# Kernel tuning notes

Hardware: AMD Instinct MI355X
Metric: run time of the kernel (lower is better)

Reference implementation:

```python
import jax, jax.numpy as jnp
import numpy as np

HID = 4096
NH = 32
NKV = 8
HD = 128
ROPE_BASE = 1000000.0
EPS = 1e-6
Q_SIZE = NH * HD      # 4096
KV_SIZE = NKV * HD    # 1024


def rms_norm(x, w):
    # x: [..., HD]
    var = jnp.mean(x * x, axis=-1, keepdims=True)
    return x * jax.lax.rsqrt(var + EPS) * w


def apply_rope(x, cos, sin):
    # x: [T, H, HD], cos/sin: [T, 1, HD//2]; neox-style rotate-half
    x1, x2 = jnp.split(x, 2, axis=-1)
    return jnp.concatenate([x1 * cos - x2 * sin, x2 * cos + x1 * sin], axis=-1)


def setup_inputs() -> dict:
    key = jax.random.key(0)
    ks = jax.random.split(key, 8)
    T = 4096
    inp = {
        "positions": jnp.arange(T, dtype=jnp.int32),
        "hidden_states": jax.random.normal(ks[0], (T, HID), dtype=jnp.float32),
        "ctx_len": 3072,
        "w_qkv": jax.random.normal(ks[1], (HID, Q_SIZE + 2 * KV_SIZE), dtype=jnp.float32) * 0.02,
        "b_qkv": jax.random.normal(ks[2], (Q_SIZE + 2 * KV_SIZE,), dtype=jnp.float32) * 0.02,
        "q_norm_w": 1.0 + 0.02 * jax.random.normal(ks[3], (HD,), dtype=jnp.float32),
        "k_norm_w": 1.0 + 0.02 * jax.random.normal(ks[4], (HD,), dtype=jnp.float32),
        "w_o": jax.random.normal(ks[5], (Q_SIZE, HID), dtype=jnp.float32) * 0.02,
    }
    return inp


def reference(positions, hidden_states, ctx_len, w_qkv, b_qkv, q_norm_w, k_norm_w, w_o):
    T = hidden_states.shape[0]
    noise_len = T - ctx_len

    qkv = hidden_states @ w_qkv + b_qkv                     # [T, 6144]
    q = qkv[:, :Q_SIZE].reshape(T, NH, HD)
    k = qkv[:, Q_SIZE:Q_SIZE + KV_SIZE].reshape(T, NKV, HD)
    v = qkv[:, Q_SIZE + KV_SIZE:].reshape(T, NKV, HD)

    # per-head RMSNorm on q and k
    q = rms_norm(q, q_norm_w)
    k = rms_norm(k, k_norm_w)

    # RoPE (neox style, full rotary dim)
    half = HD // 2
    inv_freq = 1.0 / (ROPE_BASE ** (jnp.arange(half, dtype=jnp.float32) / half))
    freqs = positions.astype(jnp.float32)[:, None] * inv_freq[None, :]   # [T, half]
    cos = jnp.cos(freqs)[:, None, :]
    sin = jnp.sin(freqs)[:, None, :]
    q = apply_rope(q, cos, sin)
    k = apply_rope(k, cos, sin)

    # Q from noise positions only; K/V from full sequence (non-causal)
    qn = q[ctx_len:]                                        # [N, NH, HD]
    g = NH // NKV
    qn = qn.reshape(noise_len, NKV, g, HD)                  # [N, kv, g, HD]
    scale = HD ** -0.5

    # scores: [kv, g, N, T] in fp32 (faithful to fp32 softmax)
    scores = jnp.einsum("nkgd,tkd->kgnt", qn, k) * scale
    probs = jax.nn.softmax(scores.astype(jnp.float32), axis=-1).astype(v.dtype)
    out = jnp.einsum("kgnt,tkd->nkgd", probs, v)            # [N, kv, g, HD]
    out = out.reshape(noise_len, NH * HD)
    return out @ w_o                                        # [N, HID]
```

## Files before the change

kernel.cpp:

```cpp
#include <hip/hip_runtime.h>
#include <stdint.h>

#define NH 32
#define NKV 8
#define HD 128
#define HID 4096
#define NQKV 6144

typedef __attribute__((ext_vector_type(8))) __bf16 bf16x8;
typedef __attribute__((ext_vector_type(4))) float f32x4;
typedef __attribute__((ext_vector_type(4))) float float4v;
typedef __attribute__((ext_vector_type(8))) unsigned short ushort8v;
typedef __attribute__((ext_vector_type(4))) unsigned short ushort4v;
typedef __attribute__((ext_vector_type(2))) unsigned short ushort2v;

__device__ __forceinline__ unsigned short f2bf(float f) {
  union { float f; unsigned u; } x; x.f = f;
  unsigned r = x.u + 0x7fffu + ((x.u >> 16) & 1u);
  return (unsigned short)(r >> 16);
}

__device__ __forceinline__ void gld16(const void* g, void* l) {
  __builtin_amdgcn_global_load_lds(
      (const __attribute__((address_space(1))) unsigned int*)g,
      (__attribute__((address_space(3))) unsigned int*)l, 16, 0, 0);
}

__device__ __forceinline__ f32x4 mfma16(bf16x8 a, bf16x8 b, f32x4 c) {
  return __builtin_amdgcn_mfma_f32_16x16x32_bf16(a, b, c, 0, 0, 0);
}

__global__ void ropetab(const int* __restrict__ pos, float* __restrict__ cosT,
                        float* __restrict__ sinT) {
  const int t = blockIdx.x, f = threadIdx.x;
  const double inv = exp(-0.2158673524681918 * (double)f);
  const double arg = (double)pos[t] * inv;
  cosT[t * 64 + f] = (float)cos(arg);
  sinT[t * 64 + f] = (float)sin(arg);
}

__global__ void convbf(const float* __restrict__ src, unsigned short* __restrict__ dst,
                       long n4) {
  long i = (long)blockIdx.x * blockDim.x + threadIdx.x;
  const long stride = (long)gridDim.x * blockDim.x;
  for (; i < n4; i += stride) {
    float4v v = *(const float4v*)(src + i * 4);
    ushort4v o;
    o.x = f2bf(v.x); o.y = f2bf(v.y); o.z = f2bf(v.z); o.w = f2bf(v.w);
    *(ushort4v*)(dst + i * 4) = o;
  }
}

__global__ __launch_bounds__(256) void wtrans(const float* __restrict__ W,
                                              unsigned short* __restrict__ Wt,
                                              int K, int N) {
  __shared__ float tile[64][65];
  const int k0 = blockIdx.y * 64, n0 = blockIdx.x * 64;
  const int tid = threadIdx.x;
  const int rk = tid >> 4, cn = (tid & 15) * 4;
#pragma unroll
  for (int rr = 0; rr < 64; rr += 16) {
    float4v v = *(const float4v*)(W + (long)(k0 + rk + rr) * N + n0 + cn);
    tile[rk + rr][cn] = v.x; tile[rk + rr][cn + 1] = v.y;
    tile[rk + rr][cn + 2] = v.z; tile[rk + rr][cn + 3] = v.w;
  }
  __syncthreads();
  const int rn = tid >> 3, ck = (tid & 7) * 8;
#pragma unroll
  for (int rr = 0; rr < 64; rr += 32) {
    ushort8v o;
#pragma unroll
    for (int j = 0; j < 8; ++j) o[j] = f2bf(tile[ck + j][rn + rr]);
    *(ushort8v*)(Wt + (long)(n0 + rn + rr) * K + k0 + ck) = o;
  }
}

__global__ __launch_bounds__(256) void vtrans(const float* __restrict__ qkv,
                                              unsigned short* __restrict__ Vt, int T) {
  __shared__ float tile[64][65];
  const int kvh = blockIdx.z;
  const int t0 = blockIdx.x * 64, d0 = blockIdx.y * 64;
  const int tid = threadIdx.x;
  const int rt = tid >> 4, cd = (tid & 15) * 4;
#pragma unroll
  for (int rr = 0; rr < 64; rr += 16) {
    float4v v = *(const float4v*)(qkv + (long)(t0 + rt + rr) * NQKV + 5120 + kvh * 128 + d0 + cd);
    tile[rt + rr][cd] = v.x; tile[rt + rr][cd + 1] = v.y;
    tile[rt + rr][cd + 2] = v.z; tile[rt + rr][cd + 3] = v.w;
  }
  __syncthreads();
  const int rd = tid >> 3, ct = (tid & 7) * 8;
#pragma unroll
  for (int rr = 0; rr < 64; rr += 32) {
    ushort8v o;
#pragma unroll
    for (int j = 0; j < 8; ++j) o[j] = f2bf(tile[ct + j][rd + rr]);
    *(ushort8v*)(Vt + ((long)kvh * 128 + d0 + rd + rr) * T + t0 + ct) = o;
  }
}

__global__ __launch_bounds__(256) void norm_rope(
    const float* __restrict__ qkv, const float* __restrict__ qw,
    const float* __restrict__ kw, const float* __restrict__ cosT,
    const float* __restrict__ sinT, unsigned short* __restrict__ Qo,
    unsigned short* __restrict__ Ko, int T, int ctx, int noise) {
  const int t = blockIdx.x;
  __shared__ float cs[64], sn[64];
  const int tid = threadIdx.x;
  if (tid < 64) { cs[tid] = cosT[t * 64 + tid]; sn[tid] = sinT[t * 64 + tid]; }
  __syncthreads();
  const int wid = tid >> 6, lane = tid & 63;
  const float* row = qkv + (long)t * NQKV;
  const bool isNoise = (t >= ctx);
  for (int sl = wid; sl < 40; sl += 4) {
    if (sl < 32 && !isNoise) continue;
    const float* x = row + sl * 128;
    float v0 = x[lane * 2], v1 = x[lane * 2 + 1];
    float ss = v0 * v0 + v1 * v1;
#pragma unroll
    for (int off = 32; off >= 1; off >>= 1) ss += __shfl_xor(ss, off);
    const float rinv = rsqrtf(ss * (1.f / 128.f) + 1e-6f);
    const float* w = (sl < 32) ? qw : kw;
    v0 *= rinv * w[lane * 2];
    v1 *= rinv * w[lane * 2 + 1];
    const float p0 = __shfl_xor(v0, 32);
    const float p1 = __shfl_xor(v1, 32);
    const int f0 = (lane * 2) & 63, f1 = (lane * 2 + 1) & 63;
    float o0, o1;
    if (lane < 32) { o0 = v0 * cs[f0] - p0 * sn[f0]; o1 = v1 * cs[f1] - p1 * sn[f1]; }
    else           { o0 = v0 * cs[f0] + p0 * sn[f0]; o1 = v1 * cs[f1] + p1 * sn[f1]; }
    ushort2v o; o.x = f2bf(o0); o.y = f2bf(o1);
    if (sl < 32)
      *(ushort2v*)(Qo + ((long)sl * noise + (t - ctx)) * 128 + lane * 2) = o;
    else
      *(ushort2v*)(Ko + ((long)(sl - 32) * T + t) * 128 + lane * 2) = o;
  }
}

__global__ __launch_bounds__(256) void gemm_qkv(
    const unsigned short* __restrict__ A, const unsigned short* __restrict__ Bt,
    float* __restrict__ C, const float* __restrict__ bias, int ctx, int nKV) {
  __shared__ unsigned short As[2][128 * 32];
  __shared__ unsigned short Bs[2][128 * 32];
  const int K = HID;
  const int tid = threadIdx.x;
  const int wid = tid >> 6, lane = tid & 63;
  const int lr = lane & 15, lg = lane >> 4;
  const int cpx = gridDim.x >> 3;
  const int swz = (blockIdx.x & 7) * cpx + (blockIdx.x >> 3);
  long bm, bn;
  if (swz < nKV) {
    bm = (long)(swz / 16) * 128;
    bn = 4096 + (long)(swz % 16) * 128;
  } else {
    const int r = swz - nKV;
    bm = ctx + (long)(r / 48) * 128;
    bn = (long)(r % 48) * 128;
  }
  const int wm = (wid >> 1) * 64;
  const int wn = (wid & 1) * 64;
  f32x4 acc[4][4] = {};

  const int r0 = (wid * 64 + lane) >> 2;
  const int ce0 = ((wid * 64 + lane) & 3) * 8;
  const int r1 = ((4 + wid) * 64 + lane) >> 2;
  const int ce1 = (((4 + wid) * 64 + lane) & 3) * 8;

#define STAGE(buf, k0)                                                        \
  do {                                                                        \
    gld16(A + (bm + r0) * (long)K + (k0) + ce0, As[buf] + wid * 512);         \
    gld16(Bt + (bn + r0) * (long)K + (k0) + ce0, Bs[buf] + wid * 512);        \
    gld16(A + (bm + r1) * (long)K + (k0) + ce1, As[buf] + (4 + wid) * 512);   \
    gld16(Bt + (bn + r1) * (long)K + (k0) + ce1, Bs[buf] + (4 + wid) * 512);  \
  } while (0)

#define COMPUTE(buf)                                                          \
  do {                                                                        \
    bf16x8 af[4], bfv[4];                                                     \
    _Pragma("unroll") for (int i = 0; i < 4; ++i) {                           \
      af[i]  = *(const bf16x8*)(As[buf] + (wm + i * 16 + lr) * 32 + lg * 8);  \
      bfv[i] = *(const bf16x8*)(Bs[buf] + (wn + i * 16 + lr) * 32 + lg * 8);  \
    }                                                                         \
    _Pragma("unroll") for (int i = 0; i < 4; ++i)                             \
      _Pragma("unroll") for (int j = 0; j < 4; ++j)                           \
        acc[i][j] = mfma16(af[i], bfv[j], acc[i][j]);                         \
  } while (0)

  STAGE(0, 0);
  __syncthreads();
  int cur = 0;
  for (int k0 = 32; k0 < K; k0 += 32) {
    STAGE(cur ^ 1, k0);
    COMPUTE(cur);
    __syncthreads();
    cur ^= 1;
  }
  COMPUTE(cur);

#pragma unroll
  for (int i = 0; i < 4; ++i) {
#pragma unroll
    for (int j = 0; j < 4; ++j) {
      const long row = bm + wm + i * 16 + lg * 4;
      const long col = bn + wn + j * 16 + lr;
      const float b = bias[col];
#pragma unroll
      for (int r = 0; r < 4; ++r)
        C[(row + r) * (long)NQKV + col] = acc[i][j][r] + b;
    }
  }
}

__global__ __launch_bounds__(256) void gemm_bt(
    const unsigned short* __restrict__ A, const unsigned short* __restrict__ Bt,
    float* __restrict__ C, int M, int N, int K) {
  __shared__ unsigned short As[2][128 * 32];
  __shared__ unsigned short Bs[2][128 * 32];
  const int tid = threadIdx.x;
  const int wid = tid >> 6, lane = tid & 63;
  const int lr = lane & 15, lg = lane >> 4;
  const long bm = (long)blockIdx.y * 128;
  const long bn = (long)blockIdx.x * 128;
  const int wm = (wid >> 1) * 64;
  const int wn = (wid & 1) * 64;
  const int kLen = K / gridDim.z;
  const int kOff = blockIdx.z * kLen;
  float* Cz = C + (size_t)blockIdx.z * M * N;
  f32x4 acc[4][4] = {};

  const int r0 = (wid * 64 + lane) >> 2;
  const int ce0 = ((wid * 64 + lane) & 3) * 8;
  const int r1 = ((4 + wid) * 64 + lane) >> 2;
  const int ce1 = (((4 + wid) * 64 + lane) & 3) * 8;

  STAGE(0, kOff);
  __syncthreads();
  int cur = 0;
  for (int k0 = kOff + 32; k0 < kOff + kLen; k0 += 32) {
    STAGE(cur ^ 1, k0);
    COMPUTE(cur);
    __syncthreads();
    cur ^= 1;
  }
  COMPUTE(cur);

#pragma unroll
  for (int i = 0; i < 4; ++i) {
#pragma unroll
    for (int j = 0; j < 4; ++j) {
      const long row = bm + wm + i * 16 + lg * 4;
      const long col = bn + wn + j * 16 + lr;
#pragma unroll
      for (int r = 0; r < 4; ++r)
        Cz[(row + r) * (long)N + col] = acc[i][j][r];
    }
  }
}

__global__ void reduce4(const float* __restrict__ P, float* __restrict__ out,
                        long n4, long stride) {
  long i = (long)blockIdx.x * blockDim.x + threadIdx.x;
  const long gs = (long)gridDim.x * blockDim.x;
  for (; i < n4; i += gs) {
    float4v a = *(const float4v*)(P + i * 4);
    float4v b = *(const float4v*)(P + stride + i * 4);
    float4v c = *(const float4v*)(P + 2 * stride + i * 4);
    float4v d = *(const float4v*)(P + 3 * stride + i * 4);
    float4v o = a + b + c + d;
    *(float4v*)(out + i * 4) = o;
  }
}

__global__ __launch_bounds__(256) void attn_kernel(
    const unsigned short* __restrict__ Q, const unsigned short* __restrict__ Kb,
    const unsigned short* __restrict__ Vt, unsigned short* __restrict__ Oout,
    int noise, int T, float scale) {
  __shared__ unsigned short Ks[64 * 128];
  __shared__ unsigned short Vs[128 * 64];
  __shared__ unsigned short Ps[4 * 16 * 64];
  const int h = blockIdx.y;
  const int kvh = h >> 2;
  const int tid = threadIdx.x, wid = tid >> 6, lane = tid & 63;
  const int lr = lane & 15, lg = lane >> 4;
  const unsigned short* qb = Q + ((long)h * noise + blockIdx.x * 64 + wid * 16 + lr) * 128;
  bf16x8 qf[4];
#pragma unroll
  for (int kc = 0; kc < 4; ++kc) qf[kc] = *(const bf16x8*)(qb + kc * 32 + lg * 8);
  const unsigned short* kbase = Kb + (long)kvh * T * 128;
  const unsigned short* vbase = Vt + (long)kvh * 128 * T;
  f32x4 accO[8] = {};
  float m_r[4], l_r[4];
#pragma unroll
  for (int r = 0; r < 4; ++r) { m_r[r] = -1e30f; l_r[r] = 0.f; }
  unsigned short* pw = Ps + wid * 1024;
  const int sw = (lr & 7) << 3;
  for (int t0 = 0; t0 < T; t0 += 64) {
#pragma unroll
    for (int c = 0; c < 4; ++c) {
      const int q = c * 4 + wid;
      const int idx = q * 64 + lane;
      const int kgi = (idx & ~7) | ((idx ^ (idx >> 4)) & 7);
      gld16(kbase + (long)t0 * 128 + (long)kgi * 8, Ks + q * 512);
      const int d = idx >> 3;
      const int cg = (idx ^ d) & 7;
      gld16(vbase + (long)d * T + t0 + cg * 8, Vs + q * 512);
    }
    __syncthreads();
    f32x4 s[4] = {};
    __builtin_amdgcn_s_setprio(1);
#pragma unroll
    for (int kc = 0; kc < 4; ++kc)
#pragma unroll
      for (int nt = 0; nt < 4; ++nt) {
        bf16x8 kf = *(const bf16x8*)(Ks + (nt * 16 + lr) * 128 + (((kc * 32) + lg * 8) ^ sw));
        s[nt] = mfma16(qf[kc], kf, s[nt]);
      }
    __builtin_amdgcn_s_setprio(0);
#pragma unroll
    for (int nt = 0; nt < 4; ++nt)
#pragma unroll
      for (int r = 0; r < 4; ++r) s[nt][r] *= scale;
    float mt[4], rs[4];
#pragma unroll
    for (int r = 0; r < 4; ++r)
      mt[r] = fmaxf(fmaxf(s[0][r], s[1][r]), fmaxf(s[2][r], s[3][r]));
#pragma unroll
    for (int off = 8; off >= 1; off >>= 1)
#pragma unroll
      for (int r = 0; r < 4; ++r) mt[r] = fmaxf(mt[r], __shfl_xor(mt[r], off));
    float corr[4];
#pragma unroll
    for (int r = 0; r < 4; ++r) {
      const float mn = fmaxf(m_r[r], mt[r]);
      corr[r] = __expf(m_r[r] - mn);
      m_r[r] = mn;
      rs[r] = 0.f;
    }
#pragma unroll
    for (int nt = 0; nt < 4; ++nt)
#pragma unroll
      for (int r = 0; r < 4; ++r) {
        const float p = __expf(s[nt][r] - m_r[r]);
        s[nt][r] = p;
        rs[r] += p;
      }
#pragma unroll
    for (int off = 8; off >= 1; off >>= 1)
#pragma unroll
      for (int r = 0; r < 4; ++r) rs[r] += __shfl_xor(rs[r], off);
#pragma unroll
    for (int r = 0; r < 4; ++r) l_r[r] = l_r[r] * corr[r] + rs[r];
#pragma unroll
    for (int nd = 0; nd < 8; ++nd)
#pragma unroll
      for (int r = 0; r < 4; ++r) accO[nd][r] *= corr[r];
#pragma unroll
    for (int nt = 0; nt < 4; ++nt)
#pragma unroll
      for (int r = 0; r < 4; ++r) {
        const int prow = lg * 4 + r;
        pw[prow * 64 + ((nt * 16 + lr) ^ ((prow & 7) << 3))] = f2bf(s[nt][r]);
      }
    __syncthreads();
    __builtin_amdgcn_s_setprio(1);
#pragma unroll
    for (int kc = 0; kc < 2; ++kc) {
      bf16x8 pa = *(const bf16x8*)(pw + lr * 64 + (((kc * 32) + lg * 8) ^ sw));
#pragma unroll
      for (int nd = 0; nd < 8; ++nd) {
        bf16x8 vf = *(const bf16x8*)(Vs + (nd * 16 + lr) * 64 + (((kc * 32) + lg * 8) ^ sw));
        accO[nd] = mfma16(pa, vf, accO[nd]);
      }
    }
    __builtin_amdgcn_s_setprio(0);
    __syncthreads();
  }
  float inv[4];
#pragma unroll
  for (int r = 0; r < 4; ++r) inv[r] = 1.f / l_r[r];
  const long orow = (long)blockIdx.x * 64 + wid * 16;
#pragma unroll
  for (int nd = 0; nd < 8; ++nd)
#pragma unroll
    for (int r = 0; r < 4; ++r)
      Oout[(orow + lg * 4 + r) * 4096 + h * 128 + nd * 16 + lr] =
          f2bf(accO[nd][r] * inv[r]);
}

extern "C" void kernel_launch(void* const* d_in, const int* in_sizes, int n_in,
                              void* d_out, int out_size, void* d_ws, size_t ws_size,
                              hipStream_t stream) {
  const int*   positions = (const int*)d_in[0];
  const float* hidden    = (const float*)d_in[1];
  const float* w_qkv     = (const float*)d_in[3];
  const float* b_qkv     = (const float*)d_in[4];
  const float* q_norm_w  = (const float*)d_in[5];
  const float* k_norm_w  = (const float*)d_in[6];
  const float* w_o       = (const float*)d_in[7];
  float* out = (float*)d_out;
  const int T = in_sizes[0];
  const int noise = out_size / HID;
  const int ctx = T - noise;

  char* ws = (char*)d_ws;
  float* qkv_f32 = (float*)ws;
  unsigned short* attn_out = (unsigned short*)ws;
  float* Cpart = (float*)(ws + (size_t)16 * 1024 * 1024);
  size_t off = (size_t)T * NQKV * 4;
  unsigned short* Hbf = (unsigned short*)(ws + off);
  unsigned short* WoT = Hbf;
  off += (size_t)T * HID * 2;
  unsigned short* WqkvT = (unsigned short*)(ws + off);
  off += (size_t)NQKV * HID * 2;
  float* cosT = (float*)(ws + off); off += (size_t)T * 64 * 4;
  float* sinT = (float*)(ws + off); off += (size_t)T * 64 * 4;
  unsigned short* Qb  = (unsigned short*)(ws + off); off += (size_t)NH * noise * HD * 2;
  unsigned short* Kbf = (unsigned short*)(ws + off); off += (size_t)NKV * T * HD * 2;
  unsigned short* Vtb = (unsigned short*)(ws + off); off += (size_t)NKV * HD * T * 2;

  ropetab<<<dim3(T), dim3(64), 0, stream>>>(positions, cosT, sinT);
  convbf<<<dim3(2048), dim3(256), 0, stream>>>(hidden, Hbf, (long)T * HID / 4);
  wtrans<<<dim3(NQKV / 64, HID / 64), dim3(256), 0, stream>>>(w_qkv, WqkvT, HID, NQKV);
  const int nKV = (2048 / 128) * (ctx / 128);
  const int nNoise = (NQKV / 128) * (noise / 128);
  gemm_qkv<<<dim3(nKV + nNoise), dim3(256), 0, stream>>>(Hbf, WqkvT, qkv_f32, b_qkv, ctx, nKV);
  wtrans<<<dim3(HID / 64, HID / 64), dim3(256), 0, stream>>>(w_o, WoT, HID, HID);
  norm_rope<<<dim3(T), dim3(256), 0, stream>>>(qkv_f32, q_norm_w, k_norm_w, cosT, sinT, Qb, Kbf, T, ctx, noise);
  vtrans<<<dim3(T / 64, HD / 64, NKV), dim3(256), 0, stream>>>(qkv_f32, Vtb, T);
  const float scale = 0.08838834764831845f;
  attn_kernel<<<dim3(noise / 64, NH), dim3(256), 0, stream>>>(Qb, Kbf, Vtb, attn_out, noise, T, scale);
  gemm_bt<<<dim3(HID / 128, noise / 128, 4), dim3(256), 0, stream>>>(attn_out, WoT, Cpart, noise, HID, HID);
  reduce4<<<dim3(1024), dim3(256), 0, stream>>>(Cpart, out, (long)noise * HID / 4, (long)noise * HID);
}
```

Baseline: 643.5 us.

## Split attention KV range across two blocks, fold scale into Q, lazy rescale

The attention kernel now splits the key/value sequence into two halves (grid z=2). It writes unnormalized fp32 partial outputs plus running max/sum, and a new combine kernel merges them into bf16. The softmax scale and log2(e) are folded into Q during norm_rope so the kernel can use exp2f without a per-score multiply. Rescaling of the accumulator is skipped when the running max grows by at most 8 (in log2 units). The split doubles the block count (16x32 = 512 before) to improve occupancy, at the cost of an extra fp32 partial write, a combine pass and slightly different bf16 rounding of Q.

After: 672.7 us. 4.5% more time.

```diff
diff --git a/kernel.cpp b/kernel.cpp
--- a/kernel.cpp
+++ b/kernel.cpp
@@ -13,6 +13,8 @@
 typedef __attribute__((ext_vector_type(8))) unsigned short ushort8v;
 typedef __attribute__((ext_vector_type(4))) unsigned short ushort4v;
 typedef __attribute__((ext_vector_type(2))) unsigned short ushort2v;
+
+#define QSCALE 0.12751744f
 
 __device__ __forceinline__ unsigned short f2bf(float f) {
   union { float f; unsigned u; } x; x.f = f;
@@ -129,11 +131,14 @@
     float o0, o1;
     if (lane < 32) { o0 = v0 * cs[f0] - p0 * sn[f0]; o1 = v1 * cs[f1] - p1 * sn[f1]; }
     else           { o0 = v0 * cs[f0] + p0 * sn[f0]; o1 = v1 * cs[f1] + p1 * sn[f1]; }
-    ushort2v o; o.x = f2bf(o0); o.y = f2bf(o1);
-    if (sl < 32)
+    ushort2v o;
+    if (sl < 32) {
+      o.x = f2bf(o0 * QSCALE); o.y = f2bf(o1 * QSCALE);
       *(ushort2v*)(Qo + ((long)sl * noise + (t - ctx)) * 128 + lane * 2) = o;
-    else
+    } else {
+      o.x = f2bf(o0); o.y = f2bf(o1);
       *(ushort2v*)(Ko + ((long)(sl - 32) * T + t) * 128 + lane * 2) = o;
+    }
   }
 }
 
@@ -273,8 +278,8 @@
 
 __global__ __launch_bounds__(256) void attn_kernel(
     const unsigned short* __restrict__ Q, const unsigned short* __restrict__ Kb,
-    const unsigned short* __restrict__ Vt, unsigned short* __restrict__ Oout,
-    int noise, int T, float scale) {
+    const unsigned short* __restrict__ Vt, float* __restrict__ Opart,
+    float2* __restrict__ ml, int noise, int T) {
   __shared__ unsigned short Ks[64 * 128];
   __shared__ unsigned short Vs[128 * 64];
   __shared__ unsigned short Ps[4 * 16 * 64];
@@ -282,6 +287,8 @@
   const int kvh = h >> 2;
   const int tid = threadIdx.x, wid = tid >> 6, lane = tid & 63;
   const int lr = lane & 15, lg = lane >> 4;
+  const int TL = T >> 1;
+  const int tBeg = blockIdx.z * TL;
   const unsigned short* qb = Q + ((long)h * noise + blockIdx.x * 64 + wid * 16 + lr) * 128;
   bf16x8 qf[4];
 #pragma unroll
@@ -294,7 +301,7 @@
   for (int r = 0; r < 4; ++r) { m_r[r] = -1e30f; l_r[r] = 0.f; }
   unsigned short* pw = Ps + wid * 1024;
   const int sw = (lr & 7) << 3;
-  for (int t0 = 0; t0 < T; t0 += 64) {
+  for (int t0 = tBeg; t0 < tBeg + TL; t0 += 64) {
 #pragma unroll
     for (int c = 0; c < 4; ++c) {
       const int q = c * 4 + wid;
@@ -316,10 +323,6 @@
         s[nt] = mfma16(qf[kc], kf, s[nt]);
       }
     __builtin_amdgcn_s_setprio(0);
-#pragma unroll
-    for (int nt = 0; nt < 4; ++nt)
-#pragma unroll
-      for (int r = 0; r < 4; ++r) s[nt][r] *= scale;
     float mt[4], rs[4];
 #pragma unroll
     for (int r = 0; r < 4; ++r)
@@ -328,19 +331,27 @@
     for (int off = 8; off >= 1; off >>= 1)
 #pragma unroll
       for (int r = 0; r < 4; ++r) mt[r] = fmaxf(mt[r], __shfl_xor(mt[r], off));
-    float corr[4];
-#pragma unroll
-    for (int r = 0; r < 4; ++r) {
-      const float mn = fmaxf(m_r[r], mt[r]);
-      corr[r] = __expf(m_r[r] - mn);
-      m_r[r] = mn;
-      rs[r] = 0.f;
-    }
+    float need = mt[0] - m_r[0];
+#pragma unroll
+    for (int r = 1; r < 4; ++r) need = fmaxf(need, mt[r] - m_r[r]);
+    if (!__all(need <= 8.f)) {
+#pragma unroll
+      for (int r = 0; r < 4; ++r) {
+        const float mn = fmaxf(m_r[r], mt[r]);
+        const float corr = exp2f(m_r[r] - mn);
+        m_r[r] = mn;
+        l_r[r] *= corr;
+#pragma unroll
+        for (int nd = 0; nd < 8; ++nd) accO[nd][r] *= corr;
+      }
+    }
+#pragma unroll
+    for (int r = 0; r < 4; ++r) rs[r] = 0.f;
 #pragma unroll
     for (int nt = 0; nt < 4; ++nt)
 #pragma unroll
       for (int r = 0; r < 4; ++r) {
-        const float p = __expf(s[nt][r] - m_r[r]);
+        const float p = exp2f(s[nt][r] - m_r[r]);
         s[nt][r] = p;
         rs[r] += p;
       }
@@ -349,11 +360,7 @@
 #pragma unroll
       for (int r = 0; r < 4; ++r) rs[r] += __shfl_xor(rs[r], off);
 #pragma unroll
-    for (int r = 0; r < 4; ++r) l_r[r] = l_r[r] * corr[r] + rs[r];
-#pragma unroll
-    for (int nd = 0; nd < 8; ++nd)
-#pragma unroll
-      for (int r = 0; r < 4; ++r) accO[nd][r] *= corr[r];
+    for (int r = 0; r < 4; ++r) l_r[r] += rs[r];
 #pragma unroll
     for (int nt = 0; nt < 4; ++nt)
 #pragma unroll
@@ -375,16 +382,38 @@
     __builtin_amdgcn_s_setprio(0);
     __syncthreads();
   }
-  float inv[4];
-#pragma unroll
-  for (int r = 0; r < 4; ++r) inv[r] = 1.f / l_r[r];
   const long orow = (long)blockIdx.x * 64 + wid * 16;
+  const long pbase = ((long)(blockIdx.z * NH + h) * noise + orow);
 #pragma unroll
   for (int nd = 0; nd < 8; ++nd)
 #pragma unroll
     for (int r = 0; r < 4; ++r)
-      Oout[(orow + lg * 4 + r) * 4096 + h * 128 + nd * 16 + lr] =
-          f2bf(accO[nd][r] * inv[r]);
+      Opart[(pbase + lg * 4 + r) * HD + nd * 16 + lr] = accO[nd][r];
+  if (lr == 0) {
+#pragma unroll
+    for (int r = 0; r < 4; ++r)
+      ml[pbase + lg * 4 + r] = make_float2(m_r[r], l_r[r]);
+  }
+}
+
+__global__ void attn_combine(const float* __restrict__ Op, const float2* __restrict__ ml,
+                             unsigned short* __restrict__ out, int noise) {
+  const long i = (long)blockIdx.x * blockDim.x + threadIdx.x;
+  const int d2 = (int)(i & 63);
+  const long hq = i >> 6;
+  const int q = (int)(hq % noise), h = (int)(hq / noise);
+  const long stride = (long)NH * noise;
+  const float2 a = *(const float2*)(Op + hq * HD + d2 * 2);
+  const float2 b = *(const float2*)(Op + (stride + hq) * HD + d2 * 2);
+  const float2 ml0 = ml[hq];
+  const float2 ml1 = ml[stride + hq];
+  const float M = fmaxf(ml0.x, ml1.x);
+  const float w0 = exp2f(ml0.x - M), w1 = exp2f(ml1.x - M);
+  const float inv = 1.f / (ml0.y * w0 + ml1.y * w1);
+  ushort2v o;
+  o.x = f2bf((a.x * w0 + b.x * w1) * inv);
+  o.y = f2bf((a.y * w0 + b.y * w1) * inv);
+  *(ushort2v*)(out + (long)q * 4096 + h * 128 + d2 * 2) = o;
 }
 
 extern "C" void kernel_launch(void* const* d_in, const int* in_sizes, int n_in,
@@ -405,7 +434,9 @@
   char* ws = (char*)d_ws;
   float* qkv_f32 = (float*)ws;
   unsigned short* attn_out = (unsigned short*)ws;
+  float* Opart = (float*)(ws + (size_t)16 * 1024 * 1024);
   float* Cpart = (float*)(ws + (size_t)16 * 1024 * 1024);
+  float2* mlbuf = (float2*)(ws + (size_t)56 * 1024 * 1024);
   size_t off = (size_t)T * NQKV * 4;
   unsigned short* Hbf = (unsigned short*)(ws + off);
   unsigned short* WoT = Hbf;
@@ -427,8 +458,8 @@
   wtrans<<<dim3(HID / 64, HID / 64), dim3(256), 0, stream>>>(w_o, WoT, HID, HID);
   norm_rope<<<dim3(T), dim3(256), 0, stream>>>(qkv_f32, q_norm_w, k_norm_w, cosT, sinT, Qb, Kbf, T, ctx, noise);
   vtrans<<<dim3(T / 64, HD / 64, NKV), dim3(256), 0, stream>>>(qkv_f32, Vtb, T);
-  const float scale = 0.08838834764831845f;
-  attn_kernel<<<dim3(noise / 64, NH), dim3(256), 0, stream>>>(Qb, Kbf, Vtb, attn_out, noise, T, scale);
+  attn_kernel<<<dim3(noise / 64, NH, 2), dim3(256), 0, stream>>>(Qb, Kbf, Vtb, Opart, mlbuf, noise, T);
+  attn_combine<<<dim3(NH * noise * 64 / 256), dim3(256), 0, stream>>>(Opart, mlbuf, attn_out, noise);
   gemm_bt<<<dim3(HID / 128, noise / 128, 4), dim3(256), 0, stream>>>(attn_out, WoT, Cpart, noise, HID, HID);
   reduce4<<<dim3(1024), dim3(256), 0, stream>>>(Cpart, out, (long)noise * HID / 4, (long)noise * HID);
 }
```
